# Performance work log

Hardware: AMD Instinct MI355X
Metric: run time of the kernel (lower is better)

Reference implementation:

```python
import jax, jax.numpy as jnp
import numpy as np

H = 1024
NH = 16
DH = H // NH
I = 4096
EPS = 1e-6


def _rms(x, g):
    # RMSNorm: x * rsqrt(mean(x^2, -1) + eps) * g
    return x * jax.lax.rsqrt(jnp.mean(x * x, axis=-1, keepdims=True) + EPS) * g


def _squash(v):
    # norm^2/(1+norm^2)/norm * v == norm/(1+norm^2) * v
    n = jnp.sqrt(jnp.sum(v * v, axis=-1, keepdims=True))
    return v * n / (1.0 + n * n)


def setup_inputs() -> dict:
    key = jax.random.key(0)
    ks = jax.random.split(key, 16)
    B, S = 4, 1024
    w = lambda k, sh: (jax.random.normal(k, sh, jnp.float32) * 0.02)
    inp = {
        "x": jax.random.normal(ks[0], (B, S, H), jnp.float32),
        "y": jax.random.normal(ks[1], (B, S, H), jnp.float32),
        "mask": jnp.zeros((B, 1, 1, S), jnp.float32),
        "Wq": w(ks[2], (H, H)), "bq": jnp.zeros((H,), jnp.float32),
        "Wk": w(ks[3], (H, H)), "bk": jnp.zeros((H,), jnp.float32),
        "Wv": w(ks[4], (H, H)), "bv": jnp.zeros((H,), jnp.float32),
        "Wo": w(ks[5], (H, H)), "bo": jnp.zeros((H,), jnp.float32),
        "g1": jnp.ones((H,), jnp.float32),
        "Wi": w(ks[6], (H, I)), "bi": jnp.zeros((I,), jnp.float32),
        "Wo2": w(ks[7], (I, H)), "bo2": jnp.zeros((H,), jnp.float32),
        "g2": jnp.ones((H,), jnp.float32),
        "t": 3,
    }
    return inp


def reference(x, y, mask, Wq, bq, Wk, bk, Wv, bv, Wo, bo, g1, Wi, bi, Wo2, bo2, g2, t):
    B, S, _ = x.shape
    # --- updRouterWt: iterative dynamic routing over t iterations ---
    b1 = b2 = None
    c1 = c2 = jnp.float32(0.5)  # softmax([0,0])
    for i in range(t):
        if i == 0:
            c1 = c2 = jnp.float32(0.5)
        else:
            bb = jnp.stack([b1, b2], axis=1)          # [B,2,S]
            cat = jax.nn.softmax(bb, axis=1)
            c1 = cat[:, 0, :, None]                   # [B,S,1]
            c2 = cat[:, 1, :, None]
        a = _squash(c1 * x + c2 * y)                  # [B,S,H]
        d1 = jnp.einsum('bsh,bsh->bs', a, x)          # diag(a @ x^T)
        d2 = jnp.einsum('bsh,bsh->bs', a, y)
        b1 = d1 if i == 0 else b1 + d1
        b2 = d2 if i == 0 else b2 + d2
    xs = c1 * x                                       # routed query stream
    ys = c2 * y                                       # routed key/value stream
    # --- cross-attention (CoAttention, dropout=0 eval) ---
    q = (xs @ Wq + bq).reshape(B, S, NH, DH).transpose(0, 2, 1, 3)
    k = (ys @ Wk + bk).reshape(B, S, NH, DH).transpose(0, 2, 1, 3)
    v = (ys @ Wv + bv).reshape(B, S, NH, DH).transpose(0, 2, 1, 3)
    scores = jnp.einsum('bhqd,bhkd->bhqk', q, k) / np.float32(np.sqrt(DH)) + mask
    probs = jax.nn.softmax(scores, axis=-1)
    ctx = jnp.einsum('bhqk,bhkd->bhqd', probs, v).transpose(0, 2, 1, 3).reshape(B, S, H)
    # BertSelfOutput_rms
    att = _rms(ctx @ Wo + bo + xs, g1)
    # BertIntermediate (exact erf gelu) + BertOutput_rms
    inter = jax.nn.gelu(att @ Wi + bi, approximate=False)
    out = _rms(inter @ Wo2 + bo2 + att, g2)
    return out
```

## Files before the change

### kernel.cpp

```cpp
#include <hip/hip_runtime.h>

typedef unsigned short u16;
typedef __attribute__((ext_vector_type(8))) short bf16x8_t;
typedef __attribute__((ext_vector_type(4))) float f32x4_t;
typedef __attribute__((ext_vector_type(4))) unsigned short u16x4_t;

#define H_DIM 1024
#define NH 16
#define DH 64
#define I_DIM 4096
#define BATCH 4
#define SEQ 1024
#define M_ROWS 4096

__device__ __forceinline__ u16 f2bf(float f) {
    unsigned int u = __builtin_bit_cast(unsigned int, f);
    u += 0x7fffu + ((u >> 16) & 1u);
    return (u16)(u >> 16);
}

__device__ __forceinline__ void gld16(const void* g, void* l) {
    __builtin_amdgcn_global_load_lds(
        (const __attribute__((address_space(1))) unsigned int*)g,
        (__attribute__((address_space(3))) unsigned int*)l,
        16, 0, 0);
}

__global__ void route_scale_kernel(const float* __restrict__ x, const float* __restrict__ y,
                                   const int* __restrict__ tptr,
                                   float* __restrict__ c1o, float* __restrict__ c2o,
                                   u16* __restrict__ xs, u16* __restrict__ ys)
{
    int tok  = blockIdx.x * 4 + (threadIdx.x >> 6);
    int lane = threadIdx.x & 63;
    const f32x4_t* xp = (const f32x4_t*)(x + (size_t)tok * H_DIM);
    const f32x4_t* yp = (const f32x4_t*)(y + (size_t)tok * H_DIM);
    f32x4_t xv[4], yv[4];
    float xx = 0.f, xy = 0.f, yy = 0.f;
#pragma unroll
    for (int k = 0; k < 4; ++k) {
        xv[k] = xp[k * 64 + lane]; yv[k] = yp[k * 64 + lane];
#pragma unroll
        for (int e = 0; e < 4; ++e) {
            xx += xv[k][e]*xv[k][e]; xy += xv[k][e]*yv[k][e]; yy += yv[k][e]*yv[k][e];
        }
    }
#pragma unroll
    for (int m = 32; m; m >>= 1) {
        xx += __shfl_xor(xx, m); xy += __shfl_xor(xy, m); yy += __shfl_xor(yy, m);
    }
    int T = tptr[0];
    float c1 = 0.5f, c2 = 0.5f, b1 = 0.f, b2 = 0.f;
    for (int i = 0; i < T; ++i) {
        if (i > 0) {
            float mx = fmaxf(b1, b2);
            float e1 = __expf(b1 - mx), e2 = __expf(b2 - mx);
            float inv = 1.0f / (e1 + e2);
            c1 = e1 * inv; c2 = e2 * inv;
        }
        float vv = c1*c1*xx + 2.0f*c1*c2*xy + c2*c2*yy;
        float n  = sqrtf(vv);
        float s  = n / (1.0f + vv);
        float d1 = s * (c1*xx + c2*xy);
        float d2 = s * (c1*xy + c2*yy);
        b1 += d1; b2 += d2;
    }
    if (lane == 0) { c1o[tok] = c1; c2o[tok] = c2; }
#pragma unroll
    for (int k = 0; k < 4; ++k) {
        u16x4_t xo, yo;
#pragma unroll
        for (int e = 0; e < 4; ++e) { xo[e] = f2bf(xv[k][e]*c1); yo[e] = f2bf(yv[k][e]*c2); }
        ((u16x4_t*)(xs + (size_t)tok * H_DIM))[k * 64 + lane] = xo;
        ((u16x4_t*)(ys + (size_t)tok * H_DIM))[k * 64 + lane] = yo;
    }
}

__global__ void pack2_kernel(const float* __restrict__ a, const float* __restrict__ b,
                             float* __restrict__ o)
{
    int i = blockIdx.x * 256 + threadIdx.x;
    o[i] = (i < 1024) ? a[i] : b[i - 1024];
}

__device__ __forceinline__ void wcast_body(const float* __restrict__ W, u16* __restrict__ Wt,
                                           int Kw, int Nw, int blk, int tid, float* t )
{
    int nbj = Nw >> 5;
    int bi = blk / nbj, bj = blk % nbj;
#pragma unroll
    for (int p = 0; p < 4; ++p) {
        int idx = p * 256 + tid;
        int r = idx >> 5, c = idx & 31;
        t[r * 33 + c] = W[(size_t)(bi*32 + r) * Nw + bj*32 + c];
    }
    __syncthreads();
#pragma unroll
    for (int p = 0; p < 4; ++p) {
        int idx = p * 256 + tid;
        int r = idx >> 5, c = idx & 31;
        Wt[(size_t)(bj*32 + r) * Kw + bi*32 + c] = f2bf(t[c * 33 + r]);
    }
}

__global__ void wcast_kernel(const float* __restrict__ W, u16* __restrict__ Wt, int Kw, int Nw)
{
    __shared__ float t[32 * 33];
    wcast_body(W, Wt, Kw, Nw, blockIdx.x, threadIdx.x, t);
}

__global__ void wcast4_kernel(const float* __restrict__ W0, const float* __restrict__ W1,
                              const float* __restrict__ W2, const float* __restrict__ W3,
                              u16* __restrict__ T0, u16* __restrict__ T1,
                              u16* __restrict__ T2, u16* __restrict__ T3)
{
    __shared__ float t[32 * 33];
    int which = blockIdx.x >> 10, blk = blockIdx.x & 1023;
    const float* W = (which == 0) ? W0 : (which == 1) ? W1 : (which == 2) ? W2 : W3;
    u16* Wt = (which == 0) ? T0 : (which == 1) ? T1 : (which == 2) ? T2 : T3;
    wcast_body(W, Wt, 1024, 1024, blk, threadIdx.x, t);
}

#define BK 64

template<int TBN>
__global__ __launch_bounds__(256, (TBN == 128) ? 3 : 4) void gemm_bt(
    const u16* __restrict__ A, const u16* __restrict__ Bt, int N, int K,
    const float* __restrict__ bias, float scale, int epi,
    u16* __restrict__ outb, float* __restrict__ outf,
    const float* __restrict__ rscale, const float* __restrict__ resm)
{
    constexpr int TBM = 128;
    constexpr int MT = (TBN == 128) ? 4 : 2;
    constexpr int NT = 4;
    __shared__ u16 As[TBM * BK];
    __shared__ u16 Bs[TBN * BK];
    const int ntN = N / TBN;
    const int tm = blockIdx.x / ntN, tn = blockIdx.x % ntN;
    const int tid = threadIdx.x;
    const int w = tid >> 6, lane = tid & 63, q4 = lane >> 4, l16 = lane & 15;
    const int wm = (TBN == 128) ? (w >> 1) * 64 : w * 32;
    const int wn = (TBN == 128) ? (w & 1) * 64 : 0;

    const int srow = tid >> 3;
    const int scol = (tid & 7) * 8;
    const u16* ga = A  + (size_t)(tm * TBM + srow) * K + scol;
    const u16* gb = Bt + (size_t)(tn * TBN + srow) * K + scol;

    f32x4_t acc[MT][NT];
#pragma unroll
    for (int mt = 0; mt < MT; ++mt)
#pragma unroll
        for (int nt = 0; nt < NT; ++nt) acc[mt][nt] = (f32x4_t){0.f,0.f,0.f,0.f};

    for (int k0 = 0; k0 < K; k0 += BK) {
        __syncthreads();
#pragma unroll
        for (int c = 0; c < 4; ++c)
            gld16(ga + (size_t)c * 32 * K + k0, &As[c * 2048 + w * 512]);
#pragma unroll
        for (int c = 0; c < TBN/32; ++c)
            gld16(gb + (size_t)c * 32 * K + k0, &Bs[c * 2048 + w * 512]);
        __syncthreads();
#pragma unroll
        for (int kc = 0; kc < 2; ++kc) {
            bf16x8_t af[MT], bfr[NT];
#pragma unroll
            for (int mt = 0; mt < MT; ++mt)
                af[mt] = *(const bf16x8_t*)&As[(wm + mt*16 + l16) * BK + kc*32 + q4*8];
#pragma unroll
            for (int nt = 0; nt < NT; ++nt)
                bfr[nt] = *(const bf16x8_t*)&Bs[(wn + nt*16 + l16) * BK + kc*32 + q4*8];
#pragma unroll
            for (int mt = 0; mt < MT; ++mt)
#pragma unroll
                for (int nt = 0; nt < NT; ++nt)
                    acc[mt][nt] = __builtin_amdgcn_mfma_f32_16x16x32_bf16(af[mt], bfr[nt], acc[mt][nt], 0, 0, 0);
        }
    }

#pragma unroll
    for (int mt = 0; mt < MT; ++mt) {
#pragma unroll
        for (int nt = 0; nt < NT; ++nt) {
            const int gcol = tn * TBN + wn + nt*16 + l16;
            const float bv = bias[gcol];
#pragma unroll
            for (int r = 0; r < 4; ++r) {
                const int grow = tm * TBM + wm + mt*16 + q4*4 + r;
                float v = acc[mt][nt][r] + bv;
                if (epi == 0) {
                    float sc2 = (gcol < 1024) ? scale : 1.0f;
                    size_t o = (size_t)(gcol >> 10) * ((size_t)M_ROWS * H_DIM)
                             + (size_t)grow * H_DIM + (gcol & 1023);
                    outb[o] = f2bf(v * sc2);
                } else if (epi == 1) {
                    const size_t oidx = (size_t)grow * N + gcol;
                    float rs = rscale ? rscale[grow] : 1.0f;
                    outf[oidx] = v + rs * resm[oidx];
                } else {
                    const size_t oidx = (size_t)grow * N + gcol;
                    float g = 0.5f * v * (1.0f + erff(v * 0.70710678118f));
                    outb[oidx] = f2bf(g);
                }
            }
        }
    }
}

__global__ void vtrans_kernel(const u16* __restrict__ vb, u16* __restrict__ vt)
{
    __shared__ u16 t[64][65];
    const int blk = blockIdx.x;
    const int st = blk & 15, h = (blk >> 4) & 15, b = blk >> 8;
    const int tid = threadIdx.x;
#pragma unroll
    for (int p = 0; p < 16; ++p) {
        int idx = p * 256 + tid;
        int s = idx >> 6, d = idx & 63;
        t[s][d] = vb[(size_t)(b*SEQ + st*64 + s) * H_DIM + h*DH + d];
    }
    __syncthreads();
#pragma unroll
    for (int p = 0; p < 16; ++p) {
        int idx = p * 256 + tid;
        int d = idx >> 6, s = idx & 63;
        vt[(size_t)((b*NH + h)*DH + d) * SEQ + st*64 + s] = t[s][d];
    }
}

__global__ __launch_bounds__(256, 3) void attn_kernel(
    const u16* __restrict__ qb, const u16* __restrict__ kb,
    const u16* __restrict__ vt, const float* __restrict__ mask,
    u16* __restrict__ ctx)
{
    __shared__ u16 plds[4][16 * 72];
    const int blk = blockIdx.x;
    const int qt = blk & 15, h = (blk >> 4) & 15, b = blk >> 8;
    const int tid = threadIdx.x, w = tid >> 6, lane = tid & 63, q4 = lane >> 4, l16 = lane & 15;

    const u16* qrow = qb + ((size_t)(b*SEQ + qt*64 + w*16 + l16) * H_DIM + h*DH);
    bf16x8_t qf0 = *(const bf16x8_t*)(qrow + q4*8);
    bf16x8_t qf1 = *(const bf16x8_t*)(qrow + 32 + q4*8);

    const u16* kbp   = kb + ((size_t)(b*SEQ) * H_DIM + h*DH);
    const u16* vbase = vt + ((size_t)((b*NH + h)*DH) * SEQ);
    const float* mrow = mask + b*SEQ;

    f32x4_t o[4];
#pragma unroll
    for (int dt = 0; dt < 4; ++dt) o[dt] = (f32x4_t){0.f,0.f,0.f,0.f};
    float mi = -1e30f, li = 0.f;
    u16* pw = &plds[w][0];

    bf16x8_t kc0[4], kc1[4], kn0[4], kn1[4];
#pragma unroll
    for (int nt = 0; nt < 4; ++nt) {
        const u16* kr = kbp + (size_t)(nt*16 + l16) * H_DIM;
        kc0[nt] = *(const bf16x8_t*)(kr + q4*8);
        kc1[nt] = *(const bf16x8_t*)(kr + 32 + q4*8);
    }

    for (int j = 0; j < 16; ++j) {
        const int kb0 = j * 64;
        bf16x8_t vf0[4], vf1[4];
#pragma unroll
        for (int dt = 0; dt < 4; ++dt) {
            const u16* vrow = vbase + (size_t)(dt*16 + l16) * SEQ + kb0;
            vf0[dt] = *(const bf16x8_t*)(vrow + q4*8);
            vf1[dt] = *(const bf16x8_t*)(vrow + 32 + q4*8);
        }
        if (j < 15) {
#pragma unroll
            for (int nt = 0; nt < 4; ++nt) {
                const u16* kr = kbp + (size_t)(kb0 + 64 + nt*16 + l16) * H_DIM;
                kn0[nt] = *(const bf16x8_t*)(kr + q4*8);
                kn1[nt] = *(const bf16x8_t*)(kr + 32 + q4*8);
            }
        }
        f32x4_t sc[4];
#pragma unroll
        for (int nt = 0; nt < 4; ++nt) {
            f32x4_t s = (f32x4_t){0.f,0.f,0.f,0.f};
            s = __builtin_amdgcn_mfma_f32_16x16x32_bf16(kc0[nt], qf0, s, 0, 0, 0);
            s = __builtin_amdgcn_mfma_f32_16x16x32_bf16(kc1[nt], qf1, s, 0, 0, 0);
            f32x4_t mv = *(const f32x4_t*)&mrow[kb0 + nt*16 + q4*4];
#pragma unroll
            for (int r = 0; r < 4; ++r) s[r] += mv[r];
            sc[nt] = s;
        }
        float tmax = sc[0][0];
#pragma unroll
        for (int nt = 0; nt < 4; ++nt)
#pragma unroll
            for (int r = 0; r < 4; ++r) tmax = fmaxf(tmax, sc[nt][r]);
        tmax = fmaxf(tmax, __shfl_xor(tmax, 16));
        tmax = fmaxf(tmax, __shfl_xor(tmax, 32));
        float nm = fmaxf(mi, tmax);
        float al = __expf(mi - nm);
        mi = nm;
        float rs = 0.f;
#pragma unroll
        for (int nt = 0; nt < 4; ++nt)
#pragma unroll
            for (int r = 0; r < 4; ++r) {
                float p = __expf(sc[nt][r] - nm);
                sc[nt][r] = p; rs += p;
            }
        rs += __shfl_xor(rs, 16);
        rs += __shfl_xor(rs, 32);
        li = li * al + rs;
#pragma unroll
        for (int dt = 0; dt < 4; ++dt)
#pragma unroll
            for (int r = 0; r < 4; ++r) o[dt][r] *= al;

#pragma unroll
        for (int nt = 0; nt < 4; ++nt) {
            u16x4_t pb;
#pragma unroll
            for (int r = 0; r < 4; ++r) pb[r] = f2bf(sc[nt][r]);
            *(u16x4_t*)&pw[l16*72 + nt*16 + q4*4] = pb;
        }
        asm volatile("s_waitcnt lgkmcnt(0)" ::: "memory");
        bf16x8_t pf0 = *(const bf16x8_t*)&pw[l16*72 + q4*8];
        bf16x8_t pf1 = *(const bf16x8_t*)&pw[l16*72 + 32 + q4*8];
#pragma unroll
        for (int dt = 0; dt < 4; ++dt) {
            o[dt] = __builtin_amdgcn_mfma_f32_16x16x32_bf16(vf0[dt], pf0, o[dt], 0, 0, 0);
            o[dt] = __builtin_amdgcn_mfma_f32_16x16x32_bf16(vf1[dt], pf1, o[dt], 0, 0, 0);
        }
        asm volatile("" ::: "memory");
#pragma unroll
        for (int nt = 0; nt < 4; ++nt) { kc0[nt] = kn0[nt]; kc1[nt] = kn1[nt]; }
    }
    const float inv = 1.0f / li;
    const size_t tokbase = (size_t)(b*SEQ + qt*64 + w*16 + l16) * H_DIM + h*DH;
#pragma unroll
    for (int dt = 0; dt < 4; ++dt) {
        u16x4_t ob;
#pragma unroll
        for (int r = 0; r < 4; ++r) ob[r] = f2bf(o[dt][r] * inv);
        *(u16x4_t*)&ctx[tokbase + dt*16 + q4*4] = ob;
    }
}

__global__ void rms_kernel(const float* __restrict__ in, const float* __restrict__ g,
                           float* __restrict__ outf, u16* __restrict__ outb)
{
    int row  = blockIdx.x * 4 + (threadIdx.x >> 6);
    int lane = threadIdx.x & 63;
    const f32x4_t* ip = (const f32x4_t*)(in + (size_t)row * H_DIM);
    f32x4_t v[4];
    float ss = 0.f;
#pragma unroll
    for (int k = 0; k < 4; ++k) {
        v[k] = ip[k * 64 + lane];
#pragma unroll
        for (int e = 0; e < 4; ++e) ss += v[k][e] * v[k][e];
    }
#pragma unroll
    for (int m = 32; m; m >>= 1) ss += __shfl_xor(ss, m);
    float sc = rsqrtf(ss * (1.0f / 1024.0f) + 1e-6f);
#pragma unroll
    for (int k = 0; k < 4; ++k) {
        f32x4_t gv = ((const f32x4_t*)g)[k * 64 + lane];
        f32x4_t ov;
        u16x4_t ob;
#pragma unroll
        for (int e = 0; e < 4; ++e) { ov[e] = v[k][e] * sc * gv[e]; ob[e] = f2bf(ov[e]); }
        if (outf) ((f32x4_t*)(outf + (size_t)row * H_DIM))[k * 64 + lane] = ov;
        if (outb) ((u16x4_t*)(outb + (size_t)row * H_DIM))[k * 64 + lane] = ob;
    }
}

extern "C" void kernel_launch(void* const* d_in, const int* in_sizes, int n_in,
                              void* d_out, int out_size, void* d_ws, size_t ws_size,
                              hipStream_t stream)
{
    const float* x   = (const float*)d_in[0];
    const float* y   = (const float*)d_in[1];
    const float* mask= (const float*)d_in[2];
    const float* Wq  = (const float*)d_in[3];
    const float* bq  = (const float*)d_in[4];
    const float* Wk  = (const float*)d_in[5];
    const float* bk  = (const float*)d_in[6];
    const float* Wv  = (const float*)d_in[7];
    const float* bv  = (const float*)d_in[8];
    const float* Wo  = (const float*)d_in[9];
    const float* bo  = (const float*)d_in[10];
    const float* g1  = (const float*)d_in[11];
    const float* Wi  = (const float*)d_in[12];
    const float* bi  = (const float*)d_in[13];
    const float* Wo2 = (const float*)d_in[14];
    const float* bo2 = (const float*)d_in[15];
    const float* g2  = (const float*)d_in[16];
    const int*   tp  = (const int*)d_in[17];
    float* out = (float*)d_out;

    char* ws = (char*)d_ws;
    const size_t MB = 1024 * 1024;
    float* c1    = (float*)(ws);
    float* c2    = (float*)(ws + 16 * 1024);
    float* bkv   = (float*)(ws + 32 * 1024);
    u16* xs_b    = (u16*)(ws + 1 * MB);
    u16* ys_b    = (u16*)(ws + 9 * MB);
    u16* wq_t    = (u16*)(ws + 17 * MB);
    u16* wk_t    = (u16*)(ws + 19 * MB);
    u16* wv_t    = (u16*)(ws + 21 * MB);
    u16* wo_t    = (u16*)(ws + 23 * MB);
    u16* wi_t    = (u16*)(ws + 25 * MB);
    u16* wo2_t   = (u16*)(ws + 33 * MB);
    u16* qb      = (u16*)(ws + 41 * MB);
    u16* kb      = (u16*)(ws + 49 * MB);
    u16* vb      = (u16*)(ws + 57 * MB);
    u16* vtb     = (u16*)(ws + 65 * MB);
    u16* inter_b = qb;
    float* attpre= (float*)(ws + 73 * MB);
    float* attf  = (float*)(ws + 89 * MB);
    (void)ws_size; (void)in_sizes; (void)n_in; (void)out_size; (void)wv_t; (void)vb;

    route_scale_kernel<<<1024, 256, 0, stream>>>(x, y, tp, c1, c2, xs_b, ys_b);
    pack2_kernel<<<8, 256, 0, stream>>>(bk, bv, bkv);
    wcast4_kernel<<<4096, 256, 0, stream>>>(Wq, Wk, Wv, Wo, wq_t, wk_t, wv_t, wo_t);
    wcast_kernel<<<4096, 256, 0, stream>>>(Wi, wi_t, 1024, 4096);
    wcast_kernel<<<4096, 256, 0, stream>>>(Wo2, wo2_t, 4096, 1024);

    gemm_bt<64><<<512, 256, 0, stream>>>(xs_b, wq_t, 1024, 1024, bq, 0.125f, 0, qb, nullptr, nullptr, nullptr);
    gemm_bt<128><<<512, 256, 0, stream>>>(ys_b, wk_t, 2048, 1024, bkv, 1.0f, 0, kb, nullptr, nullptr, nullptr);
    vtrans_kernel<<<1024, 256, 0, stream>>>(vb, vtb);
    attn_kernel<<<1024, 256, 0, stream>>>(qb, kb, vtb, mask, xs_b );
    gemm_bt<64><<<512, 256, 0, stream>>>(xs_b, wo_t, 1024, 1024, bo, 1.0f, 1, nullptr, attpre, c1, x);
    rms_kernel<<<1024, 256, 0, stream>>>(attpre, g1, attf, ys_b );
    gemm_bt<128><<<1024, 256, 0, stream>>>(ys_b, wi_t, 4096, 1024, bi, 1.0f, 2, inter_b, nullptr, nullptr, nullptr);
    gemm_bt<64><<<512, 256, 0, stream>>>(inter_b, wo2_t, 1024, 4096, bo2, 1.0f, 1, nullptr, attpre, nullptr, attf);
    rms_kernel<<<1024, 256, 0, stream>>>(attpre, g2, out, nullptr);
}
```

Before: 538.1 us.

## Stage K/V tiles in shared memory with async double buffering in attention

The attention kernel now cooperatively loads each 64x64 K and V tile into double-buffered LDS through global_load_lds, so the four waves share one copy instead of each wave fetching the full tiles from global memory into registers. Block indices are also remapped so consecutive blocks cover different batch-head pairs for the same query tile, which changes how K/V reads land in L2. The exchange is a block-wide barrier per iteration, about 33KB of extra LDS that may lower occupancy, and unswizzled LDS reads that may hit bank conflicts.

```diff
diff --git a/kernel.cpp b/kernel.cpp
--- a/kernel.cpp
+++ b/kernel.cpp
@@ -234,9 +234,15 @@
     const u16* __restrict__ vt, const float* __restrict__ mask,
     u16* __restrict__ ctx)
 {
+    __shared__ u16 Ks[2][64 * 64];
+    __shared__ u16 Vs[2][64 * 64];
     __shared__ u16 plds[4][16 * 72];
-    const int blk = blockIdx.x;
-    const int qt = blk & 15, h = (blk >> 4) & 15, b = blk >> 8;
+
+    const int raw = blockIdx.x;
+    const int xg = raw & 7, sg = raw >> 3;
+    const int bh = xg + 8 * (sg >> 4);
+    const int qt = sg & 15;
+    const int b = bh >> 4, h = bh & 15;
     const int tid = threadIdx.x, w = tid >> 6, lane = tid & 63, q4 = lane >> 4, l16 = lane & 15;
 
     const u16* qrow = qb + ((size_t)(b*SEQ + qt*64 + w*16 + l16) * H_DIM + h*DH);
@@ -247,43 +253,44 @@
     const u16* vbase = vt + ((size_t)((b*NH + h)*DH) * SEQ);
     const float* mrow = mask + b*SEQ;
 
+    const int srow0 = tid >> 3;
+    const int srow1 = 32 + (tid >> 3);
+    const int sel   = (tid & 7) * 8;
+    const int ldsb0 = w * 512;
+    const int ldsb1 = 2048 + w * 512;
+
     f32x4_t o[4];
 #pragma unroll
     for (int dt = 0; dt < 4; ++dt) o[dt] = (f32x4_t){0.f,0.f,0.f,0.f};
     float mi = -1e30f, li = 0.f;
     u16* pw = &plds[w][0];
 
-    bf16x8_t kc0[4], kc1[4], kn0[4], kn1[4];
-#pragma unroll
-    for (int nt = 0; nt < 4; ++nt) {
-        const u16* kr = kbp + (size_t)(nt*16 + l16) * H_DIM;
-        kc0[nt] = *(const bf16x8_t*)(kr + q4*8);
-        kc1[nt] = *(const bf16x8_t*)(kr + 32 + q4*8);
-    }
+    gld16(kbp + (size_t)srow0 * H_DIM + sel, &Ks[0][ldsb0]);
+    gld16(kbp + (size_t)srow1 * H_DIM + sel, &Ks[0][ldsb1]);
+    gld16(vbase + (size_t)srow0 * SEQ + sel, &Vs[0][ldsb0]);
+    gld16(vbase + (size_t)srow1 * SEQ + sel, &Vs[0][ldsb1]);
+    __syncthreads();
 
     for (int j = 0; j < 16; ++j) {
         const int kb0 = j * 64;
-        bf16x8_t vf0[4], vf1[4];
-#pragma unroll
-        for (int dt = 0; dt < 4; ++dt) {
-            const u16* vrow = vbase + (size_t)(dt*16 + l16) * SEQ + kb0;
-            vf0[dt] = *(const bf16x8_t*)(vrow + q4*8);
-            vf1[dt] = *(const bf16x8_t*)(vrow + 32 + q4*8);
-        }
+        const int buf = j & 1, nxt = buf ^ 1;
         if (j < 15) {
-#pragma unroll
-            for (int nt = 0; nt < 4; ++nt) {
-                const u16* kr = kbp + (size_t)(kb0 + 64 + nt*16 + l16) * H_DIM;
-                kn0[nt] = *(const bf16x8_t*)(kr + q4*8);
-                kn1[nt] = *(const bf16x8_t*)(kr + 32 + q4*8);
-            }
-        }
+            const u16* gK = kbp + (size_t)(kb0 + 64) * H_DIM;
+            const u16* gV = vbase + (kb0 + 64);
+            gld16(gK + (size_t)srow0 * H_DIM + sel, &Ks[nxt][ldsb0]);
+            gld16(gK + (size_t)srow1 * H_DIM + sel, &Ks[nxt][ldsb1]);
+            gld16(gV + (size_t)srow0 * SEQ + sel, &Vs[nxt][ldsb0]);
+            gld16(gV + (size_t)srow1 * SEQ + sel, &Vs[nxt][ldsb1]);
+        }
+
         f32x4_t sc[4];
 #pragma unroll
         for (int nt = 0; nt < 4; ++nt) {
+            bf16x8_t kf0 = *(const bf16x8_t*)&Ks[buf][(nt*16 + l16)*64 + q4*8];
+            bf16x8_t kf1 = *(const bf16x8_t*)&Ks[buf][(nt*16 + l16)*64 + 32 + q4*8];
             f32x4_t s = (f32x4_t){0.f,0.f,0.f,0.f};
-            s = __builtin_amdgcn_mfma_f32_16x16x32_bf16(kc0[nt], qf0, s, 0, 0, 0);
-            s = __builtin_amdgcn_mfma_f32_16x16x32_bf16(kc1[nt], qf1, s, 0, 0, 0);
+            s = __builtin_amdgcn_mfma_f32_16x16x32_bf16(kf0, qf0, s, 0, 0, 0);
+            s = __builtin_amdgcn_mfma_f32_16x16x32_bf16(kf1, qf1, s, 0, 0, 0);
             f32x4_t mv = *(const f32x4_t*)&mrow[kb0 + nt*16 + q4*4];
 #pragma unroll
             for (int r = 0; r < 4; ++r) s[r] += mv[r];
@@ -327,12 +334,12 @@
         bf16x8_t pf1 = *(const bf16x8_t*)&pw[l16*72 + 32 + q4*8];
 #pragma unroll
         for (int dt = 0; dt < 4; ++dt) {
-            o[dt] = __builtin_amdgcn_mfma_f32_16x16x32_bf16(vf0[dt], pf0, o[dt], 0, 0, 0);
-            o[dt] = __builtin_amdgcn_mfma_f32_16x16x32_bf16(vf1[dt], pf1, o[dt], 0, 0, 0);
-        }
-        asm volatile("" ::: "memory");
-#pragma unroll
-        for (int nt = 0; nt < 4; ++nt) { kc0[nt] = kn0[nt]; kc1[nt] = kn1[nt]; }
+            bf16x8_t vf0 = *(const bf16x8_t*)&Vs[buf][(dt*16 + l16)*64 + q4*8];
+            bf16x8_t vf1 = *(const bf16x8_t*)&Vs[buf][(dt*16 + l16)*64 + 32 + q4*8];
+            o[dt] = __builtin_amdgcn_mfma_f32_16x16x32_bf16(vf0, pf0, o[dt], 0, 0, 0);
+            o[dt] = __builtin_amdgcn_mfma_f32_16x16x32_bf16(vf1, pf1, o[dt], 0, 0, 0);
+        }
+        if (j < 15) __syncthreads();
     }
     const float inv = 1.0f / li;
     const size_t tokbase = (size_t)(b*SEQ + qt*64 + w*16 + l16) * H_DIM + h*DH;
```

After: 472.6 us. 1.14x faster.
